# Kernel optimization log

Hardware: AMD Instinct MI355X
Metric: run time of the kernel (lower is better)

## Reference

```python
import jax, jax.numpy as jnp
import numpy as np

EULER = 0.5772156649015329  # Euler-Mascheroni constant


def _expi_neg(t):
    """Ei(t) for t < 0, via Ei(t) = -E1(-t).

    E1 uses the power series for x < 8 and the asymptotic expansion for x >= 8.
    This replaces the scipy.special.expi CPU round-trip of the original module.
    """
    x = -t  # x > 0
    # --- series branch (x < 8): E1(x) = -gamma - ln(x) + sum_{k>=1} (-1)^{k+1} x^k/(k*k!)
    xs = jnp.minimum(x, 8.0)
    s = jnp.zeros_like(xs)
    term = xs  # (-1)^{k+1} xs^k / k!  starting at k=1
    for k in range(1, 31):
        s = s + term / k
        term = term * (-xs) / (k + 1)
    e1_small = -EULER - jnp.log(xs) + s
    # --- asymptotic branch (x >= 8): E1(x) ~ e^{-x}/x * sum_n (-1)^n n! / x^n
    xl = jnp.maximum(x, 8.0)
    a = jnp.ones_like(xl)
    acc = jnp.ones_like(xl)
    for n in range(1, 9):
        a = a * (-n) / xl
        acc = acc + a
    e1_large = jnp.exp(-xl) / xl * acc
    e1 = jnp.where(x < 8.0, e1_small, e1_large)
    return -e1


def _li(v):
    # logarithmic integral li(v) = Ei(ln v); constant w.r.t. params (scipy detaches in torch)
    return jax.lax.stop_gradient(_expi_neg(jnp.log(v)))


def _phi(u, var2, var3, var4, var5):
    log_term = jnp.log(1.0 - u)
    li_term = _li(1.0 - u)
    return (var2 / log_term
            + var3 * li_term
            + var4 * ((1.0 - u) / log_term - li_term)
            + var5 * ((1.0 - u) * (log_term + 1.0) / (2.0 * log_term ** 2) - li_term / 2.0))


def setup_inputs() -> dict:
    key = jax.random.key(0)
    B, L, D = 262144, 64, 32
    hidden = [128, 128, 64]
    ks = jax.random.split(key, 16)
    u = jax.random.uniform(ks[0], (B, L), dtype=jnp.float32, minval=1e-4, maxval=1.0 - 1e-4)
    dims = [L] + hidden + [D]
    inp = {"u": u}
    for i in range(4):
        inp[f"W{i}"] = jax.random.normal(ks[1 + 2 * i], (dims[i], dims[i + 1]), dtype=jnp.float32) / np.sqrt(dims[i]).astype(np.float32)
        inp[f"b{i}"] = jnp.zeros((dims[i + 1],), dtype=jnp.float32)
    for j in range(1, 7):
        inp[f"var{j}"] = jax.random.normal(ks[8 + j], (1, D), dtype=jnp.float32) * 0.1
    return inp


def reference(u, W0, b0, W1, b1, W2, b2, W3, b3, var1, var2, var3, var4, var5, var6):
    # MLP: three Linear+ReLU blocks then final Linear to dim_data
    h = u
    for W, b in ((W0, b0), (W1, b1), (W2, b2)):
        h = jax.nn.relu(h @ W + b)
    net = h @ W3 + b3  # (B, dim_data)
    D = net.shape[1]
    ud = u[:, :D]
    # spline corrections
    p01 = -4.0 * ud ** 5 + 5.0 * ud ** 4
    corr1 = jnp.nan_to_num(p01 * (var1 + _phi(ud, var2, var3, var4, var5)), nan=0.0)
    corr2 = var6 * (ud ** 3 - 2.0 * ud ** 2 + ud)
    net_tif = jax.nn.relu(net + corr1 + corr2)
    # inverse TIF activation: ((1 - u^2)/2)^{-x}
    return jnp.power((1.0 - ud ** 2) / 2.0, -net_tif)
```

## Files before the change

### kernel.cpp

```cpp
#include <hip/hip_runtime.h>
#include <hip/hip_bf16.h>
#include <math.h>

#define LN2_F 0.69314718055994531f
#define REGION_HALFS 2048

typedef _Float16 half8 __attribute__((ext_vector_type(8)));
typedef _Float16 h4_t __attribute__((ext_vector_type(4)));
typedef __fp16 pk2_t __attribute__((ext_vector_type(2)));
typedef __attribute__((ext_vector_type(4))) float f32x4;
typedef __attribute__((ext_vector_type(8))) short short8;

#define MFMA16(a, b, c) __builtin_amdgcn_mfma_f32_16x16x32_f16((a), (b), (c), 0, 0, 0)

__global__ void prep_weights(const float* __restrict__ W0, const float* __restrict__ W1,
                             const float* __restrict__ W2, const float* __restrict__ W3,
                             short* __restrict__ ws) {
    int e = blockIdx.x * 256 + threadIdx.x;
    const float* W; int N, NT, base, ul;
    if (e < 1024)      { W = W0; N = 128; NT = 8; base = 0;     ul = e; }
    else if (e < 3072) { W = W1; N = 128; NT = 8; base = 8192;  ul = e - 1024; }
    else if (e < 4096) { W = W2; N = 64;  NT = 4; base = 24576; ul = e - 3072; }
    else if (e < 4352) { W = W3; N = 32;  NT = 2; base = 32768; ul = e - 4096; }
    else return;
    const int cp = ul >> 6, lane = ul & 63;
    const int s = cp / NT, ct = cp % NT;
    const int k0 = s * 32 + (lane >> 4) * 8;
    const int n = ct * 16 + (lane & 15);
    union { half8 h; short8 s; } v;
#pragma unroll
    for (int j = 0; j < 8; ++j) v.h[j] = (_Float16)W[(size_t)(k0 + j) * N + n];
    *(short8*)(ws + base + cp * 512 + lane * 8) = v.s;
}


__device__ __forceinline__ void lds_fence() {
    asm volatile("s_waitcnt lgkmcnt(0)" ::: "memory");
}

__device__ __forceinline__ half8 tr_read_ks(const _Float16* region, unsigned lane_off, int s) {
    h4_t lo, hi;
    asm volatile("ds_read_b64_tr_b16 %0, %2\n\t"
                 "ds_read_b64_tr_b16 %1, %2 offset:128"
                 : "=&v"(lo), "=&v"(hi)
                 : "v"((unsigned)(uintptr_t)region + lane_off + (unsigned)(s * 1024))
                 : "memory");
    return __builtin_shufflevector(lo, hi, 0, 1, 2, 3, 4, 5, 6, 7);
}

__device__ __forceinline__ void store_tile(_Float16* __restrict__ region, int ct_global,
                                           int m, int q, f32x4 v) {
    const int base = ct_global * 256 + (m >> 2) * 64 + (m & 3) * 16 + q * 4;
    pk2_t p0 = __builtin_amdgcn_cvt_pkrtz(fmaxf(v[0], 0.0f), fmaxf(v[1], 0.0f));
    pk2_t p1 = __builtin_amdgcn_cvt_pkrtz(fmaxf(v[2], 0.0f), fmaxf(v[3], 0.0f));
    h4_t h = {(_Float16)p0[0], (_Float16)p0[1], (_Float16)p1[0], (_Float16)p1[1]};
    *(h4_t*)(region + base) = h;
}

template <int K, int N, int NEXT_NT>
__device__ __forceinline__ void layer_pipe(const half8* __restrict__ wf,
                                           const half8* __restrict__ wf_next,
                                           const float* bias, const half8 (&af)[2][4],
                                           int lane, f32x4 (&acc)[2][8],
                                           half8 (&ba)[8], half8 (&bb)[8]) {
    constexpr int NK = K / 32, NT = N / 16;
    static_assert(NK == 2 || NK == 4, "");
#pragma unroll
    for (int ct = 0; ct < NT; ++ct) {
        const float b = bias[ct];
        acc[0][ct] = f32x4{b, b, b, b};
        acc[1][ct] = f32x4{b, b, b, b};
    }
#pragma unroll
    for (int ct = 0; ct < NT; ++ct) bb[ct] = wf[(NT + ct) * 64 + lane];
#pragma unroll
    for (int ct = 0; ct < NT; ++ct) {
        acc[0][ct] = MFMA16(af[0][0], ba[ct], acc[0][ct]);
        acc[1][ct] = MFMA16(af[1][0], ba[ct], acc[1][ct]);
    }
    if constexpr (NK == 4) {
#pragma unroll
        for (int ct = 0; ct < NT; ++ct) ba[ct] = wf[(2 * NT + ct) * 64 + lane];
#pragma unroll
        for (int ct = 0; ct < NT; ++ct) {
            acc[0][ct] = MFMA16(af[0][1], bb[ct], acc[0][ct]);
            acc[1][ct] = MFMA16(af[1][1], bb[ct], acc[1][ct]);
        }
#pragma unroll
        for (int ct = 0; ct < NT; ++ct) bb[ct] = wf[(3 * NT + ct) * 64 + lane];
#pragma unroll
        for (int ct = 0; ct < NT; ++ct) {
            acc[0][ct] = MFMA16(af[0][2], ba[ct], acc[0][ct]);
            acc[1][ct] = MFMA16(af[1][2], ba[ct], acc[1][ct]);
        }
        if constexpr (NEXT_NT > 0) {
#pragma unroll
            for (int ct = 0; ct < NEXT_NT; ++ct) ba[ct] = wf_next[ct * 64 + lane];
        }
#pragma unroll
        for (int ct = 0; ct < NT; ++ct) {
            acc[0][ct] = MFMA16(af[0][3], bb[ct], acc[0][ct]);
            acc[1][ct] = MFMA16(af[1][3], bb[ct], acc[1][ct]);
        }
    } else {
        if constexpr (NEXT_NT > 0) {
#pragma unroll
            for (int ct = 0; ct < NEXT_NT; ++ct) ba[ct] = wf_next[ct * 64 + lane];
        }
#pragma unroll
        for (int ct = 0; ct < NT; ++ct) {
            acc[0][ct] = MFMA16(af[0][1], bb[ct], acc[0][ct]);
            acc[1][ct] = MFMA16(af[1][1], bb[ct], acc[1][ct]);
        }
    }
}

__global__ __launch_bounds__(256, 2) void mlp_phi_mfma(
    const float* __restrict__ u,
    const float* __restrict__ b0, const float* __restrict__ b1,
    const float* __restrict__ b2, const float* __restrict__ b3,
    const short* __restrict__ ws,
    const float* __restrict__ var1, const float* __restrict__ var2,
    const float* __restrict__ var3, const float* __restrict__ var4,
    const float* __restrict__ var5, const float* __restrict__ var6,
    float* __restrict__ out) {
    __shared__ __align__(16) _Float16 lds[4 * 2 * REGION_HALFS];
    const int t = threadIdx.x, lane = t & 63, wave = t >> 6;
    const int m = lane & 15, q = lane >> 4;
    _Float16* lw = lds + wave * 2 * REGION_HALFS;
    const unsigned lane_rd = (unsigned)(q * 256 + m * 8);
    const size_t row0 = (size_t)blockIdx.x * 128 + wave * 32;

    const half8* wf0 = (const half8*)(ws);
    const half8* wf1 = (const half8*)(ws + 8192);
    const half8* wf2 = (const half8*)(ws + 24576);
    const half8* wf3 = (const half8*)(ws + 32768);

    half8 af[2][4];
    f32x4 acc[2][8];
    half8 ba[8], bb[8];

#pragma unroll
    for (int ct = 0; ct < 8; ++ct) ba[ct] = wf0[ct * 64 + lane];
#pragma unroll
    for (int mt = 0; mt < 2; ++mt) {
        const float* up = u + (row0 + mt * 16 + m) * 64;
#pragma unroll
        for (int s = 0; s < 2; ++s) {
            float4 v0a = *(const float4*)(up + s * 32 + q * 8);
            float4 v1a = *(const float4*)(up + s * 32 + q * 8 + 4);
            pk2_t p0 = __builtin_amdgcn_cvt_pkrtz(v0a.x, v0a.y);
            pk2_t p1 = __builtin_amdgcn_cvt_pkrtz(v0a.z, v0a.w);
            pk2_t p2 = __builtin_amdgcn_cvt_pkrtz(v1a.x, v1a.y);
            pk2_t p3 = __builtin_amdgcn_cvt_pkrtz(v1a.z, v1a.w);
            af[mt][s] = half8{(_Float16)p0[0], (_Float16)p0[1], (_Float16)p1[0], (_Float16)p1[1],
                              (_Float16)p2[0], (_Float16)p2[1], (_Float16)p3[0], (_Float16)p3[1]};
        }
    }

    float bb0v[8], bb1v[8], bb2v[4], bb3v[2];
#pragma unroll
    for (int ct = 0; ct < 8; ++ct) bb0v[ct] = b0[ct * 16 + m];
#pragma unroll
    for (int ct = 0; ct < 8; ++ct) bb1v[ct] = b1[ct * 16 + m];
#pragma unroll
    for (int ct = 0; ct < 4; ++ct) bb2v[ct] = b2[ct * 16 + m];
#pragma unroll
    for (int ct = 0; ct < 2; ++ct) bb3v[ct] = b3[ct * 16 + m];

    float ev1[2], ev2[2], ev4[2], ev6[2], ev5h[2], ec3[2];
#pragma unroll
    for (int ot = 0; ot < 2; ++ot) {
        const int d = ot * 16 + m;
        ev1[ot] = var1[d]; ev2[ot] = var2[d]; ev4[ot] = var4[d]; ev6[ot] = var6[d];
        ev5h[ot] = 0.5f * var5[d];
        ec3[ot] = var3[d] - ev4[ot] - ev5h[ot];
    }

    layer_pipe<64, 128, 8>(wf0, wf1, bb0v, af, lane, acc, ba, bb);
#pragma unroll
    for (int mt = 0; mt < 2; ++mt)
#pragma unroll
        for (int ct = 0; ct < 8; ++ct)
            store_tile(lw + mt * REGION_HALFS, ct, m, q, acc[mt][ct]);
    lds_fence();
#pragma unroll
    for (int mt = 0; mt < 2; ++mt)
#pragma unroll
        for (int s = 0; s < 4; ++s) af[mt][s] = tr_read_ks(lw + mt * REGION_HALFS, lane_rd, s);
    lds_fence();
    __builtin_amdgcn_sched_barrier(0);

    layer_pipe<128, 128, 4>(wf1, wf2, bb1v, af, lane, acc, ba, bb);
#pragma unroll
    for (int mt = 0; mt < 2; ++mt)
#pragma unroll
        for (int ct = 0; ct < 8; ++ct)
            store_tile(lw + mt * REGION_HALFS, ct, m, q, acc[mt][ct]);
    lds_fence();
#pragma unroll
    for (int mt = 0; mt < 2; ++mt)
#pragma unroll
        for (int s = 0; s < 4; ++s) af[mt][s] = tr_read_ks(lw + mt * REGION_HALFS, lane_rd, s);
    lds_fence();
    __builtin_amdgcn_sched_barrier(0);

    layer_pipe<128, 64, 2>(wf2, wf3, bb2v, af, lane, acc, ba, bb);
#pragma unroll
    for (int mt = 0; mt < 2; ++mt)
#pragma unroll
        for (int ct = 0; ct < 4; ++ct)
            store_tile(lw + mt * REGION_HALFS, ct, m, q, acc[mt][ct]);
    lds_fence();
#pragma unroll
    for (int mt = 0; mt < 2; ++mt)
#pragma unroll
        for (int s = 0; s < 2; ++s) af[mt][s] = tr_read_ks(lw + mt * REGION_HALFS, lane_rd, s);

    float ue[2][8];
#pragma unroll
    for (int mt = 0; mt < 2; ++mt)
#pragma unroll
        for (int ot = 0; ot < 2; ++ot)
#pragma unroll
            for (int r = 0; r < 4; ++r)
                ue[mt][ot * 4 + r] = u[(row0 + mt * 16 + q * 4 + r) * 64 + ot * 16 + m];

    lds_fence();
    __builtin_amdgcn_sched_barrier(0);

    layer_pipe<64, 32, 0>(wf3, nullptr, bb3v, af, lane, acc, ba, bb);

#pragma unroll
    for (int ot = 0; ot < 2; ++ot) {
        const int d = ot * 16 + m;
        const float v1 = ev1[ot], v2 = ev2[ot], v4 = ev4[ot], v6 = ev6[ot];
        const float v5h = ev5h[ot];
        const float c3 = ec3[ot];
#pragma unroll
        for (int mt = 0; mt < 2; ++mt) {
#pragma unroll
            for (int r = 0; r < 4; ++r) {
                const size_t row = row0 + mt * 16 + q * 4 + r;
                const float net = acc[mt][ot][r];
                const float ud = ue[mt][ot * 4 + r];

                const float omu = 1.0f - ud;
                const float lt = __log2f(omu) * LN2_F;
                const float x = -lt;

                const float e1s = -__log2f(x) * LN2_F
                    + (-0.57721566f + x * (0.99999193f + x * (-0.24991055f
                    + x * (0.05519968f + x * (-0.00976004f + x * 0.00107857f)))));
                const float num = 0.2677737343f + x * (8.6347608925f + x * (18.0590169730f
                    + x * (8.5733287401f + x)));
                const float den = 3.9584969228f + x * (21.0996530827f + x * (25.6329561486f
                    + x * (9.5733223454f + x)));
                const float e1l = __expf(-x) * num * __builtin_amdgcn_rcpf(x * den);
                const float li = -((x < 1.0f) ? e1s : e1l);

                const float rl = __builtin_amdgcn_rcpf(lt);
                const float phi = fmaf(v4, omu, v2) * rl
                                + (v5h * omu * (lt + 1.0f)) * rl * rl
                                + c3 * li;

                const float ud2 = ud * ud;
                const float ud4 = ud2 * ud2;
                const float p01 = ud4 * fmaf(-4.0f, ud, 5.0f);
                const float corr1 = p01 * (v1 + phi);
                const float d1 = ud - 1.0f;
                const float corr2 = v6 * ud * d1 * d1;

                const float nt = fmaxf(net + corr1 + corr2, 0.0f);
                const float base = fmaf(-0.5f, ud2, 0.5f);
                out[row * 32 + d] = __builtin_amdgcn_exp2f(-nt * __log2f(base));
            }
        }
    }
}

extern "C" void kernel_launch(void* const* d_in, const int* in_sizes, int n_in,
                              void* d_out, int out_size, void* d_ws, size_t ws_size,
                              hipStream_t stream) {
    const float* u    = (const float*)d_in[0];
    const float* W0   = (const float*)d_in[1];
    const float* b0   = (const float*)d_in[2];
    const float* W1   = (const float*)d_in[3];
    const float* b1   = (const float*)d_in[4];
    const float* W2   = (const float*)d_in[5];
    const float* b2   = (const float*)d_in[6];
    const float* W3   = (const float*)d_in[7];
    const float* b3   = (const float*)d_in[8];
    const float* var1 = (const float*)d_in[9];
    const float* var2 = (const float*)d_in[10];
    const float* var3 = (const float*)d_in[11];
    const float* var4 = (const float*)d_in[12];
    const float* var5 = (const float*)d_in[13];
    const float* var6 = (const float*)d_in[14];
    float* out = (float*)d_out;
    short* ws = (short*)d_ws;

    prep_weights<<<dim3(17), dim3(256), 0, stream>>>(W0, W1, W2, W3, ws);

    const int B = in_sizes[0] / 64;
    const int blocks = B / 128;
    mlp_phi_mfma<<<dim3(blocks), dim3(256), 0, stream>>>(
        u, b0, b1, b2, b3, ws,
        var1, var2, var3, var4, var5, var6, out);
}
```

Baseline: 155.2 us.

## Split MLP layers into column halves to cut registers and raise occupancy

Replaces the software-pipelined layer routine, which double-buffered full weight-fragment sets across layers, with a simpler per-half routine that computes at most four output tiles at a time and loads weights just before use. Bias, var and u epilogue values are loaded where they are needed rather than held across the kernel. Launch bounds go from 2 to 4 blocks per CU to use the lower register footprint. The cost is that the cross-layer weight prefetch is gone, so global weight load latency is less hidden, and relies on extra waves to cover it.

```diff
diff --git a/kernel.cpp b/kernel.cpp
--- a/kernel.cpp
+++ b/kernel.cpp
@@ -57,65 +57,31 @@
     *(h4_t*)(region + base) = h;
 }
 
-template <int K, int N, int NEXT_NT>
-__device__ __forceinline__ void layer_pipe(const half8* __restrict__ wf,
-                                           const half8* __restrict__ wf_next,
-                                           const float* bias, const half8 (&af)[2][4],
-                                           int lane, f32x4 (&acc)[2][8],
-                                           half8 (&ba)[8], half8 (&bb)[8]) {
-    constexpr int NK = K / 32, NT = N / 16;
-    static_assert(NK == 2 || NK == 4, "");
-#pragma unroll
-    for (int ct = 0; ct < NT; ++ct) {
-        const float b = bias[ct];
-        acc[0][ct] = f32x4{b, b, b, b};
-        acc[1][ct] = f32x4{b, b, b, b};
-    }
-#pragma unroll
-    for (int ct = 0; ct < NT; ++ct) bb[ct] = wf[(NT + ct) * 64 + lane];
-#pragma unroll
-    for (int ct = 0; ct < NT; ++ct) {
-        acc[0][ct] = MFMA16(af[0][0], ba[ct], acc[0][ct]);
-        acc[1][ct] = MFMA16(af[1][0], ba[ct], acc[1][ct]);
-    }
-    if constexpr (NK == 4) {
-#pragma unroll
-        for (int ct = 0; ct < NT; ++ct) ba[ct] = wf[(2 * NT + ct) * 64 + lane];
-#pragma unroll
-        for (int ct = 0; ct < NT; ++ct) {
-            acc[0][ct] = MFMA16(af[0][1], bb[ct], acc[0][ct]);
-            acc[1][ct] = MFMA16(af[1][1], bb[ct], acc[1][ct]);
+template <int NK, int NT, int NC>
+__device__ __forceinline__ void layer_half(const half8* __restrict__ wf,
+                                           const float* __restrict__ bias, int ct0,
+                                           const half8 (&af)[2][4], int lane, int m,
+                                           f32x4 (&acc)[2][4]) {
+#pragma unroll
+    for (int c = 0; c < NC; ++c) {
+        const float b = bias[(ct0 + c) * 16 + m];
+        acc[0][c] = f32x4{b, b, b, b};
+        acc[1][c] = f32x4{b, b, b, b};
+    }
+#pragma unroll
+    for (int s = 0; s < NK; ++s) {
+        half8 bf[4];
+#pragma unroll
+        for (int c = 0; c < NC; ++c) bf[c] = wf[(s * NT + ct0 + c) * 64 + lane];
+#pragma unroll
+        for (int c = 0; c < NC; ++c) {
+            acc[0][c] = MFMA16(af[0][s], bf[c], acc[0][c]);
+            acc[1][c] = MFMA16(af[1][s], bf[c], acc[1][c]);
         }
-#pragma unroll
-        for (int ct = 0; ct < NT; ++ct) bb[ct] = wf[(3 * NT + ct) * 64 + lane];
-#pragma unroll
-        for (int ct = 0; ct < NT; ++ct) {
-            acc[0][ct] = MFMA16(af[0][2], ba[ct], acc[0][ct]);
-            acc[1][ct] = MFMA16(af[1][2], ba[ct], acc[1][ct]);
-        }
-        if constexpr (NEXT_NT > 0) {
-#pragma unroll
-            for (int ct = 0; ct < NEXT_NT; ++ct) ba[ct] = wf_next[ct * 64 + lane];
-        }
-#pragma unroll
-        for (int ct = 0; ct < NT; ++ct) {
-            acc[0][ct] = MFMA16(af[0][3], bb[ct], acc[0][ct]);
-            acc[1][ct] = MFMA16(af[1][3], bb[ct], acc[1][ct]);
-        }
-    } else {
-        if constexpr (NEXT_NT > 0) {
-#pragma unroll
-            for (int ct = 0; ct < NEXT_NT; ++ct) ba[ct] = wf_next[ct * 64 + lane];
-        }
-#pragma unroll
-        for (int ct = 0; ct < NT; ++ct) {
-            acc[0][ct] = MFMA16(af[0][1], bb[ct], acc[0][ct]);
-            acc[1][ct] = MFMA16(af[1][1], bb[ct], acc[1][ct]);
-        }
-    }
-}
-
-__global__ __launch_bounds__(256, 2) void mlp_phi_mfma(
+    }
+}
+
+__global__ __launch_bounds__(256, 4) void mlp_phi_mfma(
     const float* __restrict__ u,
     const float* __restrict__ b0, const float* __restrict__ b1,
     const float* __restrict__ b2, const float* __restrict__ b3,
@@ -137,11 +103,8 @@
     const half8* wf3 = (const half8*)(ws + 32768);
 
     half8 af[2][4];
-    f32x4 acc[2][8];
-    half8 ba[8], bb[8];
-
-#pragma unroll
-    for (int ct = 0; ct < 8; ++ct) ba[ct] = wf0[ct * 64 + lane];
+    f32x4 acc[2][4];
+
 #pragma unroll
     for (int mt = 0; mt < 2; ++mt) {
         const float* up = u + (row0 + mt * 16 + m) * 64;
@@ -158,92 +121,73 @@
         }
     }
 
-    float bb0v[8], bb1v[8], bb2v[4], bb3v[2];
-#pragma unroll
-    for (int ct = 0; ct < 8; ++ct) bb0v[ct] = b0[ct * 16 + m];
-#pragma unroll
-    for (int ct = 0; ct < 8; ++ct) bb1v[ct] = b1[ct * 16 + m];
-#pragma unroll
-    for (int ct = 0; ct < 4; ++ct) bb2v[ct] = b2[ct * 16 + m];
-#pragma unroll
-    for (int ct = 0; ct < 2; ++ct) bb3v[ct] = b3[ct * 16 + m];
-
-    float ev1[2], ev2[2], ev4[2], ev6[2], ev5h[2], ec3[2];
+#pragma unroll
+    for (int h = 0; h < 2; ++h) {
+        layer_half<2, 8, 4>(wf0, b0, h * 4, af, lane, m, acc);
+#pragma unroll
+        for (int mt = 0; mt < 2; ++mt)
+#pragma unroll
+            for (int c = 0; c < 4; ++c)
+                store_tile(lw + mt * REGION_HALFS, h * 4 + c, m, q, acc[mt][c]);
+    }
+    lds_fence();
+#pragma unroll
+    for (int mt = 0; mt < 2; ++mt)
+#pragma unroll
+        for (int s = 0; s < 4; ++s) af[mt][s] = tr_read_ks(lw + mt * REGION_HALFS, lane_rd, s);
+    lds_fence();
+    __builtin_amdgcn_sched_barrier(0);
+
+#pragma unroll
+    for (int h = 0; h < 2; ++h) {
+        layer_half<4, 8, 4>(wf1, b1, h * 4, af, lane, m, acc);
+#pragma unroll
+        for (int mt = 0; mt < 2; ++mt)
+#pragma unroll
+            for (int c = 0; c < 4; ++c)
+                store_tile(lw + mt * REGION_HALFS, h * 4 + c, m, q, acc[mt][c]);
+    }
+    lds_fence();
+#pragma unroll
+    for (int mt = 0; mt < 2; ++mt)
+#pragma unroll
+        for (int s = 0; s < 4; ++s) af[mt][s] = tr_read_ks(lw + mt * REGION_HALFS, lane_rd, s);
+    lds_fence();
+    __builtin_amdgcn_sched_barrier(0);
+
+    layer_half<4, 4, 4>(wf2, b2, 0, af, lane, m, acc);
+#pragma unroll
+    for (int mt = 0; mt < 2; ++mt)
+#pragma unroll
+        for (int c = 0; c < 4; ++c)
+            store_tile(lw + mt * REGION_HALFS, c, m, q, acc[mt][c]);
+    lds_fence();
+#pragma unroll
+    for (int mt = 0; mt < 2; ++mt)
+#pragma unroll
+        for (int s = 0; s < 2; ++s) af[mt][s] = tr_read_ks(lw + mt * REGION_HALFS, lane_rd, s);
+    lds_fence();
+    __builtin_amdgcn_sched_barrier(0);
+
+    layer_half<2, 2, 2>(wf3, b3, 0, af, lane, m, acc);
+
 #pragma unroll
     for (int ot = 0; ot < 2; ++ot) {
         const int d = ot * 16 + m;
-        ev1[ot] = var1[d]; ev2[ot] = var2[d]; ev4[ot] = var4[d]; ev6[ot] = var6[d];
-        ev5h[ot] = 0.5f * var5[d];
-        ec3[ot] = var3[d] - ev4[ot] - ev5h[ot];
-    }
-
-    layer_pipe<64, 128, 8>(wf0, wf1, bb0v, af, lane, acc, ba, bb);
-#pragma unroll
-    for (int mt = 0; mt < 2; ++mt)
-#pragma unroll
-        for (int ct = 0; ct < 8; ++ct)
-            store_tile(lw + mt * REGION_HALFS, ct, m, q, acc[mt][ct]);
-    lds_fence();
-#pragma unroll
-    for (int mt = 0; mt < 2; ++mt)
-#pragma unroll
-        for (int s = 0; s < 4; ++s) af[mt][s] = tr_read_ks(lw + mt * REGION_HALFS, lane_rd, s);
-    lds_fence();
-    __builtin_amdgcn_sched_barrier(0);
-
-    layer_pipe<128, 128, 4>(wf1, wf2, bb1v, af, lane, acc, ba, bb);
-#pragma unroll
-    for (int mt = 0; mt < 2; ++mt)
-#pragma unroll
-        for (int ct = 0; ct < 8; ++ct)
-            store_tile(lw + mt * REGION_HALFS, ct, m, q, acc[mt][ct]);
-    lds_fence();
-#pragma unroll
-    for (int mt = 0; mt < 2; ++mt)
-#pragma unroll
-        for (int s = 0; s < 4; ++s) af[mt][s] = tr_read_ks(lw + mt * REGION_HALFS, lane_rd, s);
-    lds_fence();
-    __builtin_amdgcn_sched_barrier(0);
-
-    layer_pipe<128, 64, 2>(wf2, wf3, bb2v, af, lane, acc, ba, bb);
-#pragma unroll
-    for (int mt = 0; mt < 2; ++mt)
-#pragma unroll
-        for (int ct = 0; ct < 4; ++ct)
-            store_tile(lw + mt * REGION_HALFS, ct, m, q, acc[mt][ct]);
-    lds_fence();
-#pragma unroll
-    for (int mt = 0; mt < 2; ++mt)
-#pragma unroll
-        for (int s = 0; s < 2; ++s) af[mt][s] = tr_read_ks(lw + mt * REGION_HALFS, lane_rd, s);
-
-    float ue[2][8];
-#pragma unroll
-    for (int mt = 0; mt < 2; ++mt)
-#pragma unroll
-        for (int ot = 0; ot < 2; ++ot)
+        const float v1 = var1[d], v2 = var2[d], v4 = var4[d], v6 = var6[d];
+        const float v5h = 0.5f * var5[d];
+        const float c3 = var3[d] - v4 - v5h;
+#pragma unroll
+        for (int mt = 0; mt < 2; ++mt) {
+            float ue[4];
 #pragma unroll
             for (int r = 0; r < 4; ++r)
-                ue[mt][ot * 4 + r] = u[(row0 + mt * 16 + q * 4 + r) * 64 + ot * 16 + m];
-
-    lds_fence();
-    __builtin_amdgcn_sched_barrier(0);
-
-    layer_pipe<64, 32, 0>(wf3, nullptr, bb3v, af, lane, acc, ba, bb);
-
-#pragma unroll
-    for (int ot = 0; ot < 2; ++ot) {
-        const int d = ot * 16 + m;
-        const float v1 = ev1[ot], v2 = ev2[ot], v4 = ev4[ot], v6 = ev6[ot];
-        const float v5h = ev5h[ot];
-        const float c3 = ec3[ot];
-#pragma unroll
-        for (int mt = 0; mt < 2; ++mt) {
+                ue[r] = u[(row0 + mt * 16 + q * 4 + r) * 64 + d];
 #pragma unroll
             for (int r = 0; r < 4; ++r) {
                 const size_t row = row0 + mt * 16 + q * 4 + r;
                 const float net = acc[mt][ot][r];
-                const float ud = ue[mt][ot * 4 + r];
+                const float ud = ue[r];
 
                 const float omu = 1.0f - ud;
                 const float lt = __log2f(omu) * LN2_F;
```

Measured after the change: 150.1 us. 1.03x faster.
